# Performance work log

Hardware: AMD Instinct MI355X
Metric: run time of the kernel (lower is better)

Reference implementation:

```python
import jax, jax.numpy as jnp
import numpy as np

N = 100000      # num_nodes
E = 1600000     # num_edges
F_IN = 5        # in_features
H = 64          # hidden_channels
HC = H // 2     # classifier hidden
L = 3           # num GCN layers
EPS = 1e-5      # BatchNorm eps


def setup_inputs() -> dict:
    key = jax.random.key(0)
    ks = jax.random.split(key, 12)
    s = 0.1
    return {
        "x": jax.random.normal(ks[0], (N, F_IN), dtype=jnp.float32),
        "edge_index": jax.random.randint(ks[1], (2, E), 0, N, dtype=jnp.int32),
        "W_in": jax.random.normal(ks[2], (F_IN, H), dtype=jnp.float32) * s,
        "b_in": jax.random.normal(ks[3], (H,), dtype=jnp.float32) * s,
        "conv_W": jax.random.normal(ks[4], (L, H, H), dtype=jnp.float32) * s,
        "conv_b": jax.random.normal(ks[5], (L, H), dtype=jnp.float32) * s,
        "bn_gamma": jnp.ones((L, H), dtype=jnp.float32),
        "bn_beta": jnp.zeros((L, H), dtype=jnp.float32),
        "W1": jax.random.normal(ks[6], (H, HC), dtype=jnp.float32) * s,
        "b1": jax.random.normal(ks[7], (HC,), dtype=jnp.float32) * s,
        "W2": jax.random.normal(ks[8], (HC, 1), dtype=jnp.float32) * s,
        "b2": jax.random.normal(ks[9], (1,), dtype=jnp.float32) * s,
    }


def reference(x, edge_index, W_in, b_in, conv_W, conv_b, bn_gamma, bn_beta, W1, b1, W2, b2):
    src, dst = edge_index[0], edge_index[1]

    # input projection + ReLU
    h = jax.nn.relu(x @ W_in + b_in)  # (N, H)

    # GCN symmetric normalization with self-loops (PyG GCNConv default):
    # deg includes the self-loop weight of 1.
    deg = jax.ops.segment_sum(jnp.ones((E,), dtype=h.dtype), dst, num_segments=N) + 1.0
    dinv = jax.lax.rsqrt(deg)                       # deg^{-1/2}, (N,)
    edge_coef = dinv[src] * dinv[dst]               # (E,)
    self_coef = dinv * dinv                         # (N,)

    for i in range(L):
        hw = h @ conv_W[i]                          # linear (no bias yet), (N, H)
        # gather -> scale -> scatter-add aggregation, plus self-loop term
        agg = jax.ops.segment_sum(hw[src] * edge_coef[:, None], dst, num_segments=N)
        agg = agg + hw * self_coef[:, None] + conv_b[i]
        # BatchNorm1d over nodes (batch statistics; eval dropout = identity)
        mean = jnp.mean(agg, axis=0)
        var = jnp.var(agg, axis=0)
        h = bn_gamma[i] * (agg - mean) * jax.lax.rsqrt(var + EPS) + bn_beta[i]
        h = jax.nn.relu(h)

    # classifier MLP: H -> H//2 -> 1, squeeze to (N,)
    logits = (jax.nn.relu(h @ W1 + b1) @ W2 + b2).squeeze(-1)
    return logits
```

## Files before the change

### kernel.cpp

```cpp
#include <hip/hip_runtime.h>

#define NN 100000
#define EE 1600000
#define EPSV 1e-5f

using short8 = __attribute__((ext_vector_type(8))) short;
using floatx4 = __attribute__((ext_vector_type(4))) float;

__device__ __forceinline__ unsigned short f2bf(float f) {
    union { float f; unsigned int u; } cv;
    cv.f = f;
    unsigned int u = cv.u;
    u += 0x7FFFu + ((u >> 16) & 1u);
    return (unsigned short)(u >> 16);
}

__device__ __forceinline__ float bf2f(unsigned short u) {
    union { unsigned int i; float f; } cv;
    cv.i = ((unsigned int)u) << 16;
    return cv.f;
}

__global__ void deg_kernel(const int* __restrict__ dst, int* __restrict__ degi8) {
    int e = blockIdx.x * 256 + threadIdx.x;
    if (e >= EE) return;
    int q = blockIdx.x & 7;
    atomicAdd(&degi8[q * NN + dst[e]], 1);
}

__global__ void scan1(const int* __restrict__ degi8, int* __restrict__ degi,
                      int* __restrict__ offsets, int* __restrict__ partial,
                      float* __restrict__ dinv) {
    __shared__ int sdata[256];
    int t = threadIdx.x;
    int n = blockIdx.x * 256 + t;
    int v = 0;
    if (n < NN) {
#pragma unroll
        for (int q = 0; q < 8; ++q) v += degi8[q * NN + n];
        degi[n] = v;
        dinv[n] = rsqrtf((float)v + 1.0f);
    }
    sdata[t] = v;
    __syncthreads();
    for (int off = 1; off < 256; off <<= 1) {
        int x = (t >= off) ? sdata[t - off] : 0;
        __syncthreads();
        sdata[t] += x;
        __syncthreads();
    }
    if (n < NN) offsets[n] = sdata[t] - v;
    if (t == 255) partial[blockIdx.x] = sdata[255];
}

__global__ void scan2(int* __restrict__ partial, int* __restrict__ partial_pref,
                      int nparts, float* __restrict__ stats) {
    __shared__ int sdata[512];
    int t = threadIdx.x;
    if (t < 384) stats[t] = 0.f;
    int v = (t < nparts) ? partial[t] : 0;
    sdata[t] = v;
    __syncthreads();
    for (int off = 1; off < 512; off <<= 1) {
        int x = (t >= off) ? sdata[t - off] : 0;
        __syncthreads();
        sdata[t] += x;
        __syncthreads();
    }
    if (t < nparts) partial_pref[t] = sdata[t] - v;
}

__global__ void fill_kernel(const int* __restrict__ src, const int* __restrict__ dst,
                            int* __restrict__ offsets,
                            const int* __restrict__ partial_pref,
                            const float* __restrict__ dinv,
                            int2* __restrict__ sorted) {
    int e = blockIdx.x * 256 + threadIdx.x;
    if (e >= EE) return;
    int d = dst[e];
    int s = src[e];
    int idx = partial_pref[d >> 8] + atomicAdd(&offsets[d], 1);
    int2 rec;
    rec.x = s;
    rec.y = __float_as_int(dinv[s] * dinv[d]);
    sorted[idx] = rec;
}

__global__ __launch_bounds__(256) void gemm64_bn(const float* __restrict__ in,
                                                 const float* __restrict__ x,
                                                 const float* __restrict__ Win,
                                                 const float* __restrict__ bin,
                                                 const float* __restrict__ stats,
                                                 const float* __restrict__ gamma,
                                                 const float* __restrict__ beta,
                                                 const float* __restrict__ W,
                                                 unsigned short* __restrict__ out,
                                                 int mode) {
    __shared__ __align__(16) unsigned short As[64 * 72];
    __shared__ __align__(16) unsigned short Wt[64 * 72];
    __shared__ float scale[64], shift[64];
    __shared__ float Wins[320];
    __shared__ float bins[64];
    int t = threadIdx.x;
    if (mode == 1) {
        if (t < 64) {
            const float invN = 1.0f / (float)NN;
            float mean = stats[t] * invN;
            float var = stats[64 + t] * invN - mean * mean;
            float rstd = rsqrtf(var + EPSV);
            float sc = gamma[t] * rstd;
            scale[t] = sc;
            shift[t] = beta[t] - mean * sc;
        }
    } else {
        for (int i = t; i < 320; i += 256) Wins[i] = Win[i];
        if (t < 64) bins[t] = bin[t];
    }
    for (int i = t; i < 4096; i += 256) {
        int k = i >> 6, c = i & 63;
        Wt[c * 72 + k] = f2bf(W[k * 64 + c]);
    }
    __syncthreads();
    int base = blockIdx.x * 64;
    if (mode == 1) {
        for (int i = t; i < 4096; i += 256) {
            int r = i >> 6, c = i & 63;
            float v = 0.f;
            if (base + r < NN) {
                v = in[(base + r) * 64 + c];
                v = fmaxf(v * scale[c] + shift[c], 0.f);
            }
            As[r * 72 + c] = f2bf(v);
        }
    } else {
        for (int i = t; i < 4096; i += 256) {
            int r = i >> 6, c = i & 63;
            int n = base + r;
            float v = 0.f;
            if (n < NN) {
                float acc = bins[c];
#pragma unroll
                for (int k = 0; k < 5; ++k) acc += x[n * 5 + k] * Wins[k * 64 + c];
                v = fmaxf(acc, 0.f);
            }
            As[r * 72 + c] = f2bf(v);
        }
    }
    __syncthreads();
    int wv = t >> 6;
    int lane = t & 63;
    int quad = lane >> 4;
    int mm = lane & 15;
    short8 a0 = *(const short8*)&As[(wv * 16 + mm) * 72 + quad * 8];
    short8 a1 = *(const short8*)&As[(wv * 16 + mm) * 72 + 32 + quad * 8];
#pragma unroll
    for (int ct = 0; ct < 4; ++ct) {
        short8 b0 = *(const short8*)&Wt[(ct * 16 + mm) * 72 + quad * 8];
        short8 b1 = *(const short8*)&Wt[(ct * 16 + mm) * 72 + 32 + quad * 8];
        floatx4 acc = {0.f, 0.f, 0.f, 0.f};
        acc = __builtin_amdgcn_mfma_f32_16x16x32_bf16(a0, b0, acc, 0, 0, 0);
        acc = __builtin_amdgcn_mfma_f32_16x16x32_bf16(a1, b1, acc, 0, 0, 0);
#pragma unroll
        for (int reg = 0; reg < 4; ++reg) {
            int n = base + wv * 16 + quad * 4 + reg;
            if (n < NN) out[n * 64 + ct * 16 + mm] = f2bf(acc[reg]);
        }
    }
}

__global__ __launch_bounds__(256) void agg_kernel(const uint2* __restrict__ hw64,
                                                  const int2* __restrict__ sorted,
                                                  const int* __restrict__ offsets,
                                                  const int* __restrict__ partial_pref,
                                                  const int* __restrict__ degi,
                                                  const float* __restrict__ dinv,
                                                  const float* __restrict__ b,
                                                  float* __restrict__ agg,
                                                  float* __restrict__ stats) {
    int t = threadIdx.x;
    int lane = t & 63;
    int w = t >> 6;
    int eg = lane >> 4;
    int cu = lane & 15;
    float b0 = b[4 * cu], b1v = b[4 * cu + 1], b2v = b[4 * cu + 2], b3v = b[4 * cu + 3];
    float bs0 = 0.f, bs1 = 0.f, bs2 = 0.f, bs3 = 0.f;
    float bq0 = 0.f, bq1 = 0.f, bq2 = 0.f, bq3 = 0.f;
    for (int n = blockIdx.x * 4 + w; n < NN; n += gridDim.x * 4) {
        int cnt = degi[n];
        int start = partial_pref[n >> 8] + offsets[n] - cnt;
        float a0 = 0.f, a1 = 0.f, a2 = 0.f, a3 = 0.f;
        if (eg == 0) {
            uint2 u = hw64[(unsigned)n * 16 + cu];
            float di = dinv[n];
            float sc = di * di;
            a0 = bf2f((unsigned short)(u.x & 0xffffu)) * sc + b0;
            a1 = bf2f((unsigned short)(u.x >> 16)) * sc + b1v;
            a2 = bf2f((unsigned short)(u.y & 0xffffu)) * sc + b2v;
            a3 = bf2f((unsigned short)(u.y >> 16)) * sc + b3v;
        }
        for (int base = 0; base < cnt; base += 64) {
            int m = min(64, cnt - base);
            int2 rec = make_int2(0, 0);
            if (lane < m) rec = sorted[start + base + lane];
            int k = 0;
            for (; k + 16 <= m; k += 16) {
                int e0 = k + eg, e1 = k + 4 + eg, e2 = k + 8 + eg, e3 = k + 12 + eg;
                int s0 = __shfl(rec.x, e0), s1 = __shfl(rec.x, e1);
                int s2 = __shfl(rec.x, e2), s3 = __shfl(rec.x, e3);
                uint2 u0 = hw64[(unsigned)s0 * 16 + cu];
                uint2 u1 = hw64[(unsigned)s1 * 16 + cu];
                uint2 u2 = hw64[(unsigned)s2 * 16 + cu];
                uint2 u3 = hw64[(unsigned)s3 * 16 + cu];
                float c0 = __int_as_float(__shfl(rec.y, e0));
                float c1 = __int_as_float(__shfl(rec.y, e1));
                float c2 = __int_as_float(__shfl(rec.y, e2));
                float c3 = __int_as_float(__shfl(rec.y, e3));
                a0 += bf2f((unsigned short)(u0.x & 0xffffu)) * c0;
                a1 += bf2f((unsigned short)(u0.x >> 16)) * c0;
                a2 += bf2f((unsigned short)(u0.y & 0xffffu)) * c0;
                a3 += bf2f((unsigned short)(u0.y >> 16)) * c0;
                a0 += bf2f((unsigned short)(u1.x & 0xffffu)) * c1;
                a1 += bf2f((unsigned short)(u1.x >> 16)) * c1;
                a2 += bf2f((unsigned short)(u1.y & 0xffffu)) * c1;
                a3 += bf2f((unsigned short)(u1.y >> 16)) * c1;
                a0 += bf2f((unsigned short)(u2.x & 0xffffu)) * c2;
                a1 += bf2f((unsigned short)(u2.x >> 16)) * c2;
                a2 += bf2f((unsigned short)(u2.y & 0xffffu)) * c2;
                a3 += bf2f((unsigned short)(u2.y >> 16)) * c2;
                a0 += bf2f((unsigned short)(u3.x & 0xffffu)) * c3;
                a1 += bf2f((unsigned short)(u3.x >> 16)) * c3;
                a2 += bf2f((unsigned short)(u3.y & 0xffffu)) * c3;
                a3 += bf2f((unsigned short)(u3.y >> 16)) * c3;
            }
            for (; k + 4 <= m; k += 4) {
                int e = k + eg;
                int s = __shfl(rec.x, e);
                uint2 u = hw64[(unsigned)s * 16 + cu];
                float c = __int_as_float(__shfl(rec.y, e));
                a0 += bf2f((unsigned short)(u.x & 0xffffu)) * c;
                a1 += bf2f((unsigned short)(u.x >> 16)) * c;
                a2 += bf2f((unsigned short)(u.y & 0xffffu)) * c;
                a3 += bf2f((unsigned short)(u.y >> 16)) * c;
            }
            if (k < m) {
                int e = k + eg;
                int s = __shfl(rec.x, e);
                uint2 u = hw64[(unsigned)s * 16 + cu];
                float c = __int_as_float(__shfl(rec.y, e));
                a0 += bf2f((unsigned short)(u.x & 0xffffu)) * c;
                a1 += bf2f((unsigned short)(u.x >> 16)) * c;
                a2 += bf2f((unsigned short)(u.y & 0xffffu)) * c;
                a3 += bf2f((unsigned short)(u.y >> 16)) * c;
            }
        }
        a0 += __shfl_xor(a0, 16);
        a1 += __shfl_xor(a1, 16);
        a2 += __shfl_xor(a2, 16);
        a3 += __shfl_xor(a3, 16);
        a0 += __shfl_xor(a0, 32);
        a1 += __shfl_xor(a1, 32);
        a2 += __shfl_xor(a2, 32);
        a3 += __shfl_xor(a3, 32);
        if (eg == 0) {
            float4 v = make_float4(a0, a1, a2, a3);
            *(float4*)&agg[(unsigned)n * 64 + 4 * cu] = v;
            bs0 += a0; bs1 += a1; bs2 += a2; bs3 += a3;
            bq0 += a0 * a0; bq1 += a1 * a1; bq2 += a2 * a2; bq3 += a3 * a3;
        }
    }
    __shared__ float red[2][4][64];
    if (eg == 0) {
        red[0][w][4 * cu] = bs0;
        red[0][w][4 * cu + 1] = bs1;
        red[0][w][4 * cu + 2] = bs2;
        red[0][w][4 * cu + 3] = bs3;
        red[1][w][4 * cu] = bq0;
        red[1][w][4 * cu + 1] = bq1;
        red[1][w][4 * cu + 2] = bq2;
        red[1][w][4 * cu + 3] = bq3;
    }
    __syncthreads();
    if (w == 0) {
        int c = t;
        float s = red[0][0][c] + red[0][1][c] + red[0][2][c] + red[0][3][c];
        float ss = red[1][0][c] + red[1][1][c] + red[1][2][c] + red[1][3][c];
        atomicAdd(&stats[c], s);
        atomicAdd(&stats[64 + c], ss);
    }
}

__global__ __launch_bounds__(256) void classifier(const float* __restrict__ agg,
                                                  const float* __restrict__ stats,
                                                  const float* __restrict__ gamma,
                                                  const float* __restrict__ beta,
                                                  const float* __restrict__ W1,
                                                  const float* __restrict__ b1,
                                                  const float* __restrict__ W2,
                                                  const float* __restrict__ b2,
                                                  float* __restrict__ out) {
    __shared__ float W1s[2048];
    __shared__ float b1s[32];
    __shared__ float W2s[32];
    __shared__ float scale[64], shift[64];
    int t = threadIdx.x;
    for (int i = t; i < 2048; i += 256) W1s[i] = W1[i];
    if (t < 32) {
        b1s[t] = b1[t];
        W2s[t] = W2[t];
    }
    if (t < 64) {
        const float invN = 1.0f / (float)NN;
        float mean = stats[t] * invN;
        float var = stats[64 + t] * invN - mean * mean;
        float rstd = rsqrtf(var + EPSV);
        float sc = gamma[t] * rstd;
        scale[t] = sc;
        shift[t] = beta[t] - mean * sc;
    }
    __syncthreads();
    int n = blockIdx.x * 256 + t;
    if (n >= NN) return;
    float4 h4[16];
    const float4* hp = (const float4*)(agg + n * 64);
#pragma unroll
    for (int i = 0; i < 16; ++i) h4[i] = hp[i];
    float* hr = (float*)h4;
#pragma unroll
    for (int k = 0; k < 64; ++k) hr[k] = fmaxf(hr[k] * scale[k] + shift[k], 0.f);
    float o = b2[0];
    for (int c = 0; c < 32; ++c) {
        float z = b1s[c];
#pragma unroll
        for (int k = 0; k < 64; ++k) z += hr[k] * W1s[k * 32 + c];
        o += fmaxf(z, 0.f) * W2s[c];
    }
    out[n] = o;
}

extern "C" void kernel_launch(void* const* d_in, const int* in_sizes, int n_in,
                              void* d_out, int out_size, void* d_ws, size_t ws_size,
                              hipStream_t stream) {
    const float* x    = (const float*)d_in[0];
    const int*   ei   = (const int*)d_in[1];
    const float* Win  = (const float*)d_in[2];
    const float* bin  = (const float*)d_in[3];
    const float* cW   = (const float*)d_in[4];
    const float* cb   = (const float*)d_in[5];
    const float* gam  = (const float*)d_in[6];
    const float* bet  = (const float*)d_in[7];
    const float* W1   = (const float*)d_in[8];
    const float* b1   = (const float*)d_in[9];
    const float* W2   = (const float*)d_in[10];
    const float* b2   = (const float*)d_in[11];
    float* out = (float*)d_out;

    unsigned short* hw = (unsigned short*)d_ws;
    float* agg   = (float*)d_ws + NN * 32;
    float* dinv  = agg + NN * 64;
    float* stats = dinv + NN;
    int*  degi        = (int*)(stats + 3 * 128);
    int*  offsets     = degi + NN;
    int2* sorted      = (int2*)(offsets + NN);
    int*  partial     = (int*)(sorted + EE);
    int*  partial_pref = partial + 512;
    int*  degi8       = partial_pref + 512;

    const int* src = ei;
    const int* dst = ei + EE;

    const int NB = (NN + 255) / 256;
    const int EB = (EE + 255) / 256;

    (void)hipMemsetAsync(degi8, 0, 8 * NN * sizeof(int), stream);

    deg_kernel<<<EB, 256, 0, stream>>>(dst, degi8);
    scan1<<<NB, 256, 0, stream>>>(degi8, degi, offsets, partial, dinv);
    scan2<<<1, 512, 0, stream>>>(partial, partial_pref, NB, stats);
    fill_kernel<<<EB, 256, 0, stream>>>(src, dst, offsets, partial_pref, dinv, sorted);

    for (int i = 0; i < 3; ++i) {
        gemm64_bn<<<(NN + 63) / 64, 256, 0, stream>>>(
            agg, x, Win, bin, stats + (i - 1) * 128, gam + (i - 1) * 64,
            bet + (i - 1) * 64, cW + i * 4096, hw, i > 0 ? 1 : 0);
        agg_kernel<<<2048, 256, 0, stream>>>((const uint2*)hw, sorted, offsets,
                                             partial_pref, degi, dinv, cb + i * 64, agg,
                                             stats + i * 128);
    }

    classifier<<<(NN + 255) / 256, 256, 0, stream>>>(agg, stats + 2 * 128, gam + 2 * 64,
                                                     bet + 2 * 64, W1, b1, W2, b2, out);
}
```

Measured before the change: 524.9 us.

## Pre-bin edges by destination range before CSR fill to localize scatter

The degree-count kernel now also partitions edges into 8 destination-range buckets (each split into 8 sub-streams) and writes packed (dst,src) records to a staging buffer. A new fill kernel walks each bucket so the atomic offset increments and scattered writes into the sorted edge array stay inside a narrow destination window, which should improve cache locality. The cost is an extra write and read of the edge list through staging, plus a fixed per-bucket capacity (RCAP) that could overflow if the edge distribution were skewed.

After: 583.4 us. 1.11x slower.

```diff
diff --git a/kernel.cpp b/kernel.cpp
--- a/kernel.cpp
+++ b/kernel.cpp
@@ -3,6 +3,10 @@
 #define NN 100000
 #define EE 1600000
 #define EPSV 1e-5f
+#define QW 12500
+#define NSUB 8
+#define RCAP 27008
+#define PB 16
 
 using short8 = __attribute__((ext_vector_type(8))) short;
 using floatx4 = __attribute__((ext_vector_type(4))) float;
@@ -21,11 +25,34 @@
     return cv.f;
 }
 
-__global__ void deg_kernel(const int* __restrict__ dst, int* __restrict__ degi8) {
-    int e = blockIdx.x * 256 + threadIdx.x;
-    if (e >= EE) return;
-    int q = blockIdx.x & 7;
-    atomicAdd(&degi8[q * NN + dst[e]], 1);
+__global__ void deg_bin(const int* __restrict__ src, const int* __restrict__ dst,
+                        int* __restrict__ degi8, int* __restrict__ cursors,
+                        long long* __restrict__ staging) {
+    __shared__ int bcnt[8];
+    __shared__ int bbase[8];
+    __shared__ long long recs[8 * 260];
+    int t = threadIdx.x;
+    if (t < 8) bcnt[t] = 0;
+    __syncthreads();
+    int e = blockIdx.x * 256 + t;
+    int qh = blockIdx.x & 7;
+    if (e < EE) {
+        int d = dst[e];
+        int s = src[e];
+        atomicAdd(&degi8[qh * NN + d], 1);
+        int q = (unsigned)d / (unsigned)QW;
+        int rank = atomicAdd(&bcnt[q], 1);
+        recs[q * 260 + rank] = ((long long)d << 32) | (unsigned int)s;
+    }
+    __syncthreads();
+    int sub = blockIdx.x & 7;
+    if (t < 8) bbase[t] = atomicAdd(&cursors[t * NSUB + sub], bcnt[t]);
+    __syncthreads();
+    for (int q = 0; q < 8; ++q) {
+        int c = bcnt[q];
+        long long* dp = staging + ((long long)(q * NSUB + sub) * RCAP + bbase[q]);
+        for (int i = t; i < c; i += 256) dp[i] = recs[q * 260 + i];
+    }
 }
 
 __global__ void scan1(const int* __restrict__ degi8, int* __restrict__ degi,
@@ -70,20 +97,27 @@
     if (t < nparts) partial_pref[t] = sdata[t] - v;
 }
 
-__global__ void fill_kernel(const int* __restrict__ src, const int* __restrict__ dst,
-                            int* __restrict__ offsets,
-                            const int* __restrict__ partial_pref,
-                            const float* __restrict__ dinv,
-                            int2* __restrict__ sorted) {
-    int e = blockIdx.x * 256 + threadIdx.x;
-    if (e >= EE) return;
-    int d = dst[e];
-    int s = src[e];
-    int idx = partial_pref[d >> 8] + atomicAdd(&offsets[d], 1);
-    int2 rec;
-    rec.x = s;
-    rec.y = __float_as_int(dinv[s] * dinv[d]);
-    sorted[idx] = rec;
+__global__ void binB(const long long* __restrict__ staging,
+                     const int* __restrict__ cursors,
+                     int* __restrict__ offsets,
+                     const int* __restrict__ partial_pref,
+                     const float* __restrict__ dinv,
+                     int2* __restrict__ sorted) {
+    int q = blockIdx.x & 7;
+    int sub = (blockIdx.x >> 3) & 7;
+    int part = blockIdx.x >> 6;
+    int len = cursors[q * NSUB + sub];
+    const long long* st = staging + (long long)(q * NSUB + sub) * RCAP;
+    for (int i = part * 256 + threadIdx.x; i < len; i += PB * 256) {
+        long long rv = st[i];
+        int s = (int)(unsigned int)(rv & 0xffffffffll);
+        int d = (int)(rv >> 32);
+        int idx = partial_pref[d >> 8] + atomicAdd(&offsets[d], 1);
+        int2 rec;
+        rec.x = s;
+        rec.y = __float_as_int(dinv[s] * dinv[d]);
+        sorted[idx] = rec;
+    }
 }
 
 __global__ __launch_bounds__(256) void gemm64_bn(const float* __restrict__ in,
@@ -364,6 +398,8 @@
     int*  partial     = (int*)(sorted + EE);
     int*  partial_pref = partial + 512;
     int*  degi8       = partial_pref + 512;
+    int*  cursors     = degi8 + 8 * NN;
+    long long* staging = (long long*)(cursors + 64);
 
     const int* src = ei;
     const int* dst = ei + EE;
@@ -371,12 +407,13 @@
     const int NB = (NN + 255) / 256;
     const int EB = (EE + 255) / 256;
 
-    (void)hipMemsetAsync(degi8, 0, 8 * NN * sizeof(int), stream);
-
-    deg_kernel<<<EB, 256, 0, stream>>>(dst, degi8);
+    (void)hipMemsetAsync(degi8, 0, (8 * NN + 64) * sizeof(int), stream);
+
+    deg_bin<<<EB, 256, 0, stream>>>(src, dst, degi8, cursors, staging);
     scan1<<<NB, 256, 0, stream>>>(degi8, degi, offsets, partial, dinv);
     scan2<<<1, 512, 0, stream>>>(partial, partial_pref, NB, stats);
-    fill_kernel<<<EB, 256, 0, stream>>>(src, dst, offsets, partial_pref, dinv, sorted);
+    binB<<<8 * NSUB * PB, 256, 0, stream>>>(staging, cursors, offsets, partial_pref,
+                                            dinv, sorted);
 
     for (int i = 0; i < 3; ++i) {
         gemm64_bn<<<(NN + 63) / 64, 256, 0, stream>>>(
```
